# Optimization experiments

Hardware: AMD Instinct MI355X
Metric: run time of the kernel (lower is better)

The kernel has to match this reference:

```python
import jax, jax.numpy as jnp
import numpy as np

H = 256  # hidden_dim
Z = 4    # z_dim

def gru_step(x, h, Wih, Whh, bih, bhh):
    gi = x @ Wih.T + bih            # [B, 3H]
    gh = h @ Whh.T + bhh            # [B, 3H]
    ir, iz, inn = jnp.split(gi, 3, axis=-1)
    hr, hz, hn = jnp.split(gh, 3, axis=-1)
    r = jax.nn.sigmoid(ir + hr)
    z = jax.nn.sigmoid(iz + hz)
    n = jnp.tanh(inn + r * hn)
    return (1.0 - z) * n + z * h

def gru_scan(xs, h0, Wih, Whh, bih, bhh):
    # xs: [L, B, D] time-major; returns all hidden states [L, B, H]
    def step(h, x):
        h = gru_step(x, h, Wih, Whh, bih, bhh)
        return h, h
    _, hs = jax.lax.scan(step, h0, xs)
    return hs

def feat_z(z, fz_W1, fz_b1, fz_W2, fz_b2):
    # MLPEmbedding(z_dim -> [z_dim//2] -> feature_z), Linear+tanh per layer (dropout off in eval)
    h = jnp.tanh(z @ fz_W1.T + fz_b1)
    return jnp.tanh(h @ fz_W2.T + fz_b2)

def _make_params(key):
    ks = jax.random.split(key, 32)
    s = 0.05
    p = {}
    p['fx_W'] = jax.random.normal(ks[0], (64, 1)) * s
    p['fx_b'] = jnp.zeros((64,))
    p['fz_W1'] = jax.random.normal(ks[1], (2, 4)) * s
    p['fz_b1'] = jnp.zeros((2,))
    p['fz_W2'] = jax.random.normal(ks[2], (32, 2)) * s
    p['fz_b2'] = jnp.zeros((32,))
    p['phi1_Wih'] = jax.random.normal(ks[3], (3 * H, 64)) * s
    p['phi1_Whh'] = jax.random.normal(ks[4], (3 * H, H)) * s
    p['phi1_bih'] = jnp.zeros((3 * H,))
    p['phi1_bhh'] = jnp.zeros((3 * H,))
    p['phi2_Wih'] = jax.random.normal(ks[5], (3 * H, 32)) * s
    p['phi2_Whh'] = jax.random.normal(ks[6], (3 * H, H)) * s
    p['phi2_bih'] = jnp.zeros((3 * H,))
    p['phi2_bhh'] = jnp.zeros((3 * H,))
    p['pn_locW'] = jax.random.normal(ks[7], (Z, 2 * H)) * s
    p['pn_locb'] = jnp.zeros((Z,))
    p['pn_scaleW'] = jax.random.normal(ks[8], (Z, 2 * H)) * s
    p['pn_scaleb'] = jnp.zeros((Z,))
    p['th_Wih'] = jax.random.normal(ks[9], (3 * H, 32)) * s
    p['th_Whh'] = jax.random.normal(ks[10], (3 * H, H)) * s
    p['th_bih'] = jnp.zeros((3 * H,))
    p['th_bhh'] = jnp.zeros((3 * H,))
    p['tn_locW'] = jax.random.normal(ks[11], (1, H)) * s
    p['tn_locb'] = jnp.zeros((1,))
    return p

def setup_inputs() -> dict:
    key = jax.random.key(0)
    kx, ke, kp = jax.random.split(key, 3)
    B, L = 256, 512
    inp = {
        'x': jax.random.normal(kx, (B, L, 1), dtype=jnp.float32),
        'eps': jax.random.normal(ke, (L, B, Z), dtype=jnp.float32),
    }
    inp.update(_make_params(kp))
    return inp

def reference(x, eps, fx_W, fx_b, fz_W1, fz_b1, fz_W2, fz_b2,
              phi1_Wih, phi1_Whh, phi1_bih, phi1_bhh,
              phi2_Wih, phi2_Whh, phi2_bih, phi2_bhh,
              pn_locW, pn_locb, pn_scaleW, pn_scaleb,
              th_Wih, th_Whh, th_bih, th_bhh,
              tn_locW, tn_locb):
    B, L, _ = x.shape
    # ---- encode ----
    xf = jnp.tanh(x @ fx_W.T + fx_b)                 # [B, L, 64] feature_extra_x
    xs_rev = jnp.transpose(xf[:, ::-1, :], (1, 0, 2))  # [L, B, 64] reversed, time-major
    h0 = jnp.zeros((B, H), dtype=x.dtype)
    xh = gru_scan(xs_rev, h0, phi1_Wih, phi1_Whh, phi1_bih, phi1_bhh)  # [L, B, H]
    xh_r = xh[::-1]                                  # flip back to forward time order

    def enc_step(carry, inp_t):
        zh, zf = carry
        xh_t, eps_t = inp_t
        zh = gru_step(zf, zh, phi2_Wih, phi2_Whh, phi2_bih, phi2_bhh)
        cat = jnp.concatenate([zh, xh_t], axis=-1)   # [B, 2H]
        z_loc = cat @ pn_locW.T + pn_locb
        z_scale = jax.nn.softplus(cat @ pn_scaleW.T + pn_scaleb)
        z_t = z_loc + z_scale * eps_t                # Normal sample (n_sample=1 -> mean == sample)
        zf = feat_z(z_t, fz_W1, fz_b1, fz_W2, fz_b2)
        return (zh, zf), z_t

    zf0 = jnp.zeros((B, 32), dtype=x.dtype)
    _, z_tm = jax.lax.scan(enc_step, (h0, zf0), (xh_r, eps))  # [L, B, Z]

    # ---- decode ----
    zf_seq = feat_z(z_tm, fz_W1, fz_b1, fz_W2, fz_b2)          # [L, B, 32]
    hs = gru_scan(zf_seq, h0, th_Wih, th_Whh, th_bih, th_bhh)  # [L, B, H]
    x_loc = hs @ tn_locW.T + tn_locb                           # [L, B, 1]
    return jnp.transpose(x_loc, (1, 0, 2))                     # [B, L, 1]
```

## Files before the change

kernel.cpp:

```cpp
#include <hip/hip_runtime.h>
#include <hip/hip_bf16.h>
#include <stdint.h>


struct RvaeParams {
  const float *x, *eps;
  const float *fx_W, *fx_b;
  const float *fz_W1, *fz_b1, *fz_W2, *fz_b2;
  const float *p1_Wih, *p1_Whh, *p1_bih, *p1_bhh;
  const float *p2_Wih, *p2_Whh, *p2_bih, *p2_bhh;
  const float *pn_locW, *pn_locb, *pn_scaleW, *pn_scaleb;
  const float *th_Wih, *th_Whh, *th_bih, *th_bhh;
  const float *tn_locW, *tn_locb;
  float* out;
  unsigned* ctr;
  float* hbuf;
  float* zpart;
  float* zf_seq;
  __hip_bfloat16* xh;
};

__device__ __forceinline__ float agent_load_f32(const float* p) {
  return __hip_atomic_load(p, __ATOMIC_RELAXED, __HIP_MEMORY_SCOPE_AGENT);
}
__device__ __forceinline__ void agent_store_f32(float* p, float v) {
  __hip_atomic_store(p, v, __ATOMIC_RELAXED, __HIP_MEMORY_SCOPE_AGENT);
}
__device__ __forceinline__ unsigned long long agent_load_u64(const unsigned long long* p) {
  return __hip_atomic_load(p, __ATOMIC_RELAXED, __HIP_MEMORY_SCOPE_AGENT);
}
__device__ __forceinline__ float sigm(float xx) { return 1.0f / (1.0f + __expf(-xx)); }
__device__ __forceinline__ float ftanh(float xx) { return 1.0f - 2.0f / (__expf(2.0f * xx) + 1.0f); }
__device__ __forceinline__ float softplusf(float xx) { return (xx > 15.0f) ? xx : log1pf(__expf(xx)); }

__device__ __forceinline__ void gh_part(const float* Wh, const float* hL, int b, int u,
                                        float& ar, float& az, float& an) {
  float r0 = 0.f, z0 = 0.f, n0 = 0.f;
  const float4* h4 = (const float4*)hL + b * 65;
  const float4* wr = (const float4*)Wh + u * 65;
  const float4* wz = (const float4*)Wh + (32 + u) * 65;
  const float4* wn = (const float4*)Wh + (64 + u) * 65;
#pragma unroll 4
  for (int k = 0; k < 64; ++k) {
    float4 hv = h4[k];
    float4 a = wr[k]; float4 c = wz[k]; float4 d = wn[k];
    r0 = fmaf(a.x, hv.x, r0); r0 = fmaf(a.y, hv.y, r0); r0 = fmaf(a.z, hv.z, r0); r0 = fmaf(a.w, hv.w, r0);
    z0 = fmaf(c.x, hv.x, z0); z0 = fmaf(c.y, hv.y, z0); z0 = fmaf(c.z, hv.z, z0); z0 = fmaf(c.w, hv.w, z0);
    n0 = fmaf(d.x, hv.x, n0); n0 = fmaf(d.y, hv.y, n0); n0 = fmaf(d.z, hv.z, n0); n0 = fmaf(d.w, hv.w, n0);
  }
  ar = r0; az = z0; an = n0;
}

template<int KD4>
__device__ __forceinline__ void gi_part(const float* Wi, int strideF4, const float* inL, int b, int u,
                                        float& gr, float& gz, float& gn) {
  float r0 = 0.f, z0 = 0.f, n0 = 0.f;
  const float4* i4 = (const float4*)inL + b * 17;
  const float4* wr = (const float4*)Wi + u * strideF4;
  const float4* wz = (const float4*)Wi + (32 + u) * strideF4;
  const float4* wn = (const float4*)Wi + (64 + u) * strideF4;
#pragma unroll 4
  for (int k = 0; k < KD4; ++k) {
    float4 hv = i4[k];
    float4 a = wr[k]; float4 c = wz[k]; float4 d = wn[k];
    r0 = fmaf(a.x, hv.x, r0); r0 = fmaf(a.y, hv.y, r0); r0 = fmaf(a.z, hv.z, r0); r0 = fmaf(a.w, hv.w, r0);
    z0 = fmaf(c.x, hv.x, z0); z0 = fmaf(c.y, hv.y, z0); z0 = fmaf(c.z, hv.z, z0); z0 = fmaf(c.w, hv.w, z0);
    n0 = fmaf(d.x, hv.x, n0); n0 = fmaf(d.y, hv.y, n0); n0 = fmaf(d.z, hv.z, n0); n0 = fmaf(d.w, hv.w, n0);
  }
  gr = r0; gz = z0; gn = n0;
}

extern "C" __global__ void __launch_bounds__(256, 1) rvae_main(RvaeParams P) {
  __shared__ __align__(16) float Wh[96 * 260];
  __shared__ __align__(16) float SB[7584];
  __shared__ __align__(16) float hL[8 * 260];
  __shared__ __align__(16) float inL[8 * 68];
  __shared__ float bihL[96], bhhL[96];
  __shared__ float fxwL[64], fxbL[64];
  __shared__ float fzW1L[8], fzb1L[2], fzW2L[64], fzb2L[32];
  __shared__ float pnlb[4], pnsb[4];
  __shared__ float wred[4 * 8 * 8];
  __shared__ float zred[64];
  __shared__ float ztL[32];
  __shared__ float hmL[16];
  __shared__ float oredL[4 * 8];
  __shared__ float tnwL[32];
  __shared__ unsigned bcount;

  const int tid = threadIdx.x;
  const int wgid = blockIdx.x;
  const int s = wgid >> 5;
  const int g = wgid & 31;
  const int b_l = tid & 7;
  const int u = tid >> 3;
  const int j = s * 32 + u;
  const int bg = g * 8 + b_l;
  unsigned* gctr = P.ctr + g * 16;

  if (tid < 64) { fxwL[tid] = P.fx_W[tid]; fxbL[tid] = P.fx_b[tid]; fzW2L[tid] = P.fz_W2[tid]; }
  if (tid < 8)  fzW1L[tid] = P.fz_W1[tid];
  if (tid < 2)  fzb1L[tid] = P.fz_b1[tid];
  if (tid < 32) fzb2L[tid] = P.fz_b2[tid];
  if (tid < 4)  { pnlb[tid] = P.pn_locb[tid]; pnsb[tid] = P.pn_scaleb[tid]; }
  if (tid == 0) bcount = 0;

  auto gbar = [&]() {
    __syncthreads();
    if (tid == 0) {
      unsigned target = (++bcount) * 8u;
      __hip_atomic_fetch_add(gctr, 1u, __ATOMIC_RELEASE, __HIP_MEMORY_SCOPE_AGENT);
      int guard = 0;
      while (__hip_atomic_load(gctr, __ATOMIC_ACQUIRE, __HIP_MEMORY_SCOPE_AGENT) < target) {
        __builtin_amdgcn_s_sleep(1);
        if (++guard > (1 << 27)) break;
      }
    }
    __syncthreads();
  };

  auto load_whh = [&](const float* Whh) {
    for (int rr = 0; rr < 96; ++rr) {
      int gate = rr >> 5, uu = rr & 31;
      Wh[rr * 260 + tid] = Whh[(gate * 256 + s * 32 + uu) * 256 + tid];
    }
  };
  auto load_wih32 = [&](const float* Wih) {
    for (int blk = 0; blk < 12; ++blk) {
      int rr = blk * 8 + (tid >> 5); int c = tid & 31;
      int gate = rr >> 5, uu = rr & 31;
      SB[rr * 36 + c] = Wih[(gate * 256 + s * 32 + uu) * 32 + c];
    }
  };
  auto load_bias = [&](const float* bih, const float* bhh) {
    if (tid < 96) {
      int gate = tid >> 5, uu = tid & 31;
      bihL[tid] = bih[gate * 256 + s * 32 + uu];
      bhhL[tid] = bhh[gate * 256 + s * 32 + uu];
    }
  };

  load_whh(P.p1_Whh);
  for (int blk = 0; blk < 24; ++blk) {
    int rr = blk * 4 + (tid >> 6); int c = tid & 63;
    int gate = rr >> 5, uu = rr & 31;
    SB[rr * 68 + c] = P.p1_Wih[(gate * 256 + s * 32 + uu) * 64 + c];
  }
  load_bias(P.p1_bih, P.p1_bhh);
  agent_store_f32(P.hbuf + bg * 256 + j, 0.0f);
  {
#pragma unroll
    for (int i = 0; i < 2; ++i) {
      int idx = tid + i * 256; int bb = idx >> 6, k = idx & 63;
      float xv = P.x[(size_t)(g * 8 + bb) * 512 + 511];
      inL[bb * 68 + k] = ftanh(fmaf(xv, fxwL[k], fxbL[k]));
    }
  }
  gbar();
  for (int t = 0; t < 512; ++t) {
    const float* hin = P.hbuf + (t & 1) * 65536 + g * 2048;
    float* hout = P.hbuf + ((t + 1) & 1) * 65536;
    unsigned long long hv[4];
    const unsigned long long* h64 = (const unsigned long long*)hin;
#pragma unroll
    for (int i = 0; i < 4; ++i) hv[i] = agent_load_u64(h64 + tid + i * 256);
    float gr, gz, gn;
    gi_part<16>(SB, 17, inL, b_l, u, gr, gz, gn);
#pragma unroll
    for (int i = 0; i < 4; ++i) {
      int idx = tid + i * 256; int bb = idx >> 7, kp = (idx & 127) * 2;
      union { unsigned long long q; float f[2]; } cv; cv.q = hv[i];
      hL[bb * 260 + kp] = cv.f[0]; hL[bb * 260 + kp + 1] = cv.f[1];
    }
    __syncthreads();
    float ar, az, an;
    gh_part(Wh, hL, b_l, u, ar, az, an);
    float hold = hL[b_l * 260 + j];
    float r = sigm(gr + bihL[u] + ar + bhhL[u]);
    float z = sigm(gz + bihL[32 + u] + az + bhhL[32 + u]);
    float n = ftanh(fmaf(r, an + bhhL[64 + u], gn + bihL[64 + u]));
    float hnew = fmaf(z, hold - n, n);
    int t_in = 511 - t;
    agent_store_f32(hout + bg * 256 + j, hnew);
    P.xh[((size_t)wgid * 512 + t_in) * 256 + b_l * 32 + u] = __float2bfloat16(hnew);
    if (t < 511) {
#pragma unroll
      for (int i = 0; i < 2; ++i) {
        int idx = tid + i * 256; int bb = idx >> 6, k = idx & 63;
        float xv = P.x[(size_t)(g * 8 + bb) * 512 + (t_in - 1)];
        inL[bb * 68 + k] = ftanh(fmaf(xv, fxwL[k], fxbL[k]));
      }
    }
    gbar();
  }

  __syncthreads();
  load_whh(P.p2_Whh);
  load_wih32(P.p2_Wih);
  for (int idx = tid; idx < 2048; idx += 256) {
    int o = idx >> 9, c = idx & 511;
    SB[3456 + o * 516 + c] = P.pn_locW[idx];
    SB[5520 + o * 516 + c] = P.pn_scaleW[idx];
  }
  load_bias(P.p2_bih, P.p2_bhh);
  agent_store_f32(P.hbuf + bg * 256 + j, 0.0f);
  for (int idx = tid; idx < 8 * 68; idx += 256) inL[idx] = 0.0f;
  gbar();
  for (int t = 0; t < 512; ++t) {
    const float* hin = P.hbuf + (t & 1) * 65536 + g * 2048;
    float* hout = P.hbuf + ((t + 1) & 1) * 65536;
    unsigned long long hv[4];
    const unsigned long long* h64 = (const unsigned long long*)hin;
#pragma unroll
    for (int i = 0; i < 4; ++i) hv[i] = agent_load_u64(h64 + tid + i * 256);
    float xhv = __bfloat162float(P.xh[((size_t)wgid * 512 + t) * 256 + b_l * 32 + u]);
    float gr, gz, gn;
    gi_part<8>(SB, 9, inL, b_l, u, gr, gz, gn);
#pragma unroll
    for (int i = 0; i < 4; ++i) {
      int idx = tid + i * 256; int bb = idx >> 7, kp = (idx & 127) * 2;
      union { unsigned long long q; float f[2]; } cv; cv.q = hv[i];
      hL[bb * 260 + kp] = cv.f[0]; hL[bb * 260 + kp + 1] = cv.f[1];
    }
    __syncthreads();
    float ar, az, an;
    gh_part(Wh, hL, b_l, u, ar, az, an);
    float hold = hL[b_l * 260 + j];
    float r = sigm(gr + bihL[u] + ar + bhhL[u]);
    float z = sigm(gz + bihL[32 + u] + az + bhhL[32 + u]);
    float n = ftanh(fmaf(r, an + bhhL[64 + u], gn + bihL[64 + u]));
    float hnew = fmaf(z, hold - n, n);
    agent_store_f32(hout + bg * 256 + j, hnew);
    float p[8];
#pragma unroll
    for (int o = 0; o < 4; ++o)
      p[o] = fmaf(hnew, SB[3456 + o * 516 + j], xhv * SB[3456 + o * 516 + 256 + j]);
#pragma unroll
    for (int o = 0; o < 4; ++o)
      p[4 + o] = fmaf(hnew, SB[5520 + o * 516 + j], xhv * SB[5520 + o * 516 + 256 + j]);
#pragma unroll
    for (int o = 0; o < 8; ++o) {
      float v = p[o];
      v += __shfl_down(v, 32); v += __shfl_down(v, 16); v += __shfl_down(v, 8);
      p[o] = v;
    }
    {
      int lane = tid & 63, wv = tid >> 6;
      if (lane < 8) {
#pragma unroll
        for (int o = 0; o < 8; ++o) wred[wv * 64 + lane * 8 + o] = p[o];
      }
    }
    __syncthreads();
    float* zp = P.zpart + (t & 1) * 16384 + g * 512;
    if (tid < 64) {
      int bb = tid >> 3, o = tid & 7;
      float sum = wred[bb * 8 + o] + wred[64 + bb * 8 + o] + wred[128 + bb * 8 + o] + wred[192 + bb * 8 + o];
      agent_store_f32(zp + s * 64 + bb * 8 + o, sum);
    }
    gbar();
    if (tid < 64) {
      int bb = tid >> 3, o = tid & 7;
      float sum = 0.f;
#pragma unroll
      for (int sp = 0; sp < 8; ++sp) sum += agent_load_f32(zp + sp * 64 + bb * 8 + o);
      zred[bb * 8 + o] = sum;
    }
    __syncthreads();
    if (tid < 32) {
      int bb = tid >> 2, zi = tid & 3;
      float loc = zred[bb * 8 + zi] + pnlb[zi];
      float sc = softplusf(zred[bb * 8 + 4 + zi] + pnsb[zi]);
      float e = P.eps[((size_t)t * 256 + g * 8 + bb) * 4 + zi];
      ztL[bb * 4 + zi] = fmaf(sc, e, loc);
    }
    __syncthreads();
    if (tid < 16) {
      int bb = tid >> 1, m = tid & 1;
      float a = fzb1L[m];
#pragma unroll
      for (int i = 0; i < 4; ++i) a = fmaf(ztL[bb * 4 + i], fzW1L[m * 4 + i], a);
      hmL[bb * 2 + m] = ftanh(a);
    }
    __syncthreads();
    {
      int bb = tid >> 5, o = tid & 31;
      float zf = ftanh(fmaf(hmL[bb * 2], fzW2L[o * 2], fmaf(hmL[bb * 2 + 1], fzW2L[o * 2 + 1], fzb2L[o])));
      inL[bb * 68 + o] = zf;
      if (s == 0) agent_store_f32(P.zf_seq + ((size_t)t * 256 + g * 8 + bb) * 32 + o, zf);
    }
    __syncthreads();
  }

  __syncthreads();
  load_whh(P.th_Whh);
  load_wih32(P.th_Wih);
  load_bias(P.th_bih, P.th_bhh);
  if (tid < 32) tnwL[tid] = P.tn_locW[s * 32 + tid];
  agent_store_f32(P.hbuf + bg * 256 + j, 0.0f);
  gbar();
  const float tnb = P.tn_locb[0];
  for (int t = 0; t < 512; ++t) {
    const float* hin = P.hbuf + (t & 1) * 65536 + g * 2048;
    float* hout = P.hbuf + ((t + 1) & 1) * 65536;
    unsigned long long hv[4];
    const unsigned long long* h64 = (const unsigned long long*)hin;
#pragma unroll
    for (int i = 0; i < 4; ++i) hv[i] = agent_load_u64(h64 + tid + i * 256);
    {
      int bb = tid >> 5, o = tid & 31;
      inL[bb * 68 + o] = agent_load_f32(P.zf_seq + ((size_t)t * 256 + g * 8 + bb) * 32 + o);
    }
#pragma unroll
    for (int i = 0; i < 4; ++i) {
      int idx = tid + i * 256; int bb = idx >> 7, kp = (idx & 127) * 2;
      union { unsigned long long q; float f[2]; } cv; cv.q = hv[i];
      hL[bb * 260 + kp] = cv.f[0]; hL[bb * 260 + kp + 1] = cv.f[1];
    }
    __syncthreads();
    float gr, gz, gn;
    gi_part<8>(SB, 9, inL, b_l, u, gr, gz, gn);
    float ar, az, an;
    gh_part(Wh, hL, b_l, u, ar, az, an);
    float hold = hL[b_l * 260 + j];
    float r = sigm(gr + bihL[u] + ar + bhhL[u]);
    float z = sigm(gz + bihL[32 + u] + az + bhhL[32 + u]);
    float n = ftanh(fmaf(r, an + bhhL[64 + u], gn + bihL[64 + u]));
    float hnew = fmaf(z, hold - n, n);
    agent_store_f32(hout + bg * 256 + j, hnew);
    float pv = hnew * tnwL[u];
    pv += __shfl_down(pv, 32); pv += __shfl_down(pv, 16); pv += __shfl_down(pv, 8);
    {
      int lane = tid & 63, wv = tid >> 6;
      if (lane < 8) oredL[wv * 8 + lane] = pv;
    }
    __syncthreads();
    if (tid < 8) {
      float v = oredL[tid] + oredL[8 + tid] + oredL[16 + tid] + oredL[24 + tid];
      if (s == 0) v += tnb;
      atomicAdd(P.out + (size_t)(g * 8 + tid) * 512 + t, v);
    }
    gbar();
  }
}

extern "C" void kernel_launch(void* const* d_in, const int* in_sizes, int n_in,
                              void* d_out, int out_size, void* d_ws, size_t ws_size,
                              hipStream_t stream) {
  (void)in_sizes; (void)n_in; (void)ws_size;
  RvaeParams P;
  P.x        = (const float*)d_in[0];
  P.eps      = (const float*)d_in[1];
  P.fx_W     = (const float*)d_in[2];  P.fx_b     = (const float*)d_in[3];
  P.fz_W1    = (const float*)d_in[4];  P.fz_b1    = (const float*)d_in[5];
  P.fz_W2    = (const float*)d_in[6];  P.fz_b2    = (const float*)d_in[7];
  P.p1_Wih   = (const float*)d_in[8];  P.p1_Whh   = (const float*)d_in[9];
  P.p1_bih   = (const float*)d_in[10]; P.p1_bhh   = (const float*)d_in[11];
  P.p2_Wih   = (const float*)d_in[12]; P.p2_Whh   = (const float*)d_in[13];
  P.p2_bih   = (const float*)d_in[14]; P.p2_bhh   = (const float*)d_in[15];
  P.pn_locW  = (const float*)d_in[16]; P.pn_locb  = (const float*)d_in[17];
  P.pn_scaleW= (const float*)d_in[18]; P.pn_scaleb= (const float*)d_in[19];
  P.th_Wih   = (const float*)d_in[20]; P.th_Whh   = (const float*)d_in[21];
  P.th_bih   = (const float*)d_in[22]; P.th_bhh   = (const float*)d_in[23];
  P.tn_locW  = (const float*)d_in[24]; P.tn_locb  = (const float*)d_in[25];
  P.out = (float*)d_out;
  char* ws = (char*)d_ws;
  P.ctr    = (unsigned*)ws;
  P.hbuf   = (float*)(ws + 4096);
  P.zpart  = (float*)(ws + 4096 + 524288);
  P.zf_seq = (float*)(ws + 4096 + 524288 + 131072);
  P.xh = (__hip_bfloat16*)(ws + 4096 + 524288 + 131072 + 16777216);

  hipMemsetAsync(d_out, 0, (size_t)out_size * sizeof(float), stream);
  hipMemsetAsync(d_ws, 0, 4096, stream);
  void* args[] = { (void*)&P };
  hipError_t err = hipLaunchCooperativeKernel((void*)rvae_main, dim3(256), dim3(256), args, 0, stream);
  if (err != hipSuccess) {
    hipLaunchKernelGGL(rvae_main, dim3(256), dim3(256), 0, stream, P);
  }
}
```

Baseline: 12.78 ms.

## Rewrite RVAE kernel with per-slice flag sync, 512 threads, split-K gates

Replaces the counter-based group barrier with per-slice monotonic flags that each wave polls, so the two barriers per encoder step become one publish/poll. Block size doubles to 512 with a split-K GRU matvec reduced through DPP. The encoder's cross-block z reduction is dropped: every block computes the full loc/scale projection itself from staged xh and h, lagged one step. Other changes: packed bf16 xh stores, a shared LDS pool, and overlapping the decoder output reduction with the next step. The cost is more redundant per-block work and more LDS traffic.

```diff
diff --git a/kernel.cpp b/kernel.cpp
--- a/kernel.cpp
+++ b/kernel.cpp
@@ -2,6 +2,9 @@
 #include <hip/hip_bf16.h>
 #include <stdint.h>
 
+
+#define EXTF 11840
+#define POOLF (24576 + EXTF)
 
 struct RvaeParams {
   const float *x, *eps;
@@ -13,122 +16,100 @@
   const float *th_Wih, *th_Whh, *th_bih, *th_bhh;
   const float *tn_locW, *tn_locb;
   float* out;
-  unsigned* ctr;
+  unsigned* flags;
   float* hbuf;
-  float* zpart;
   float* zf_seq;
-  __hip_bfloat16* xh;
+  unsigned* xh;
 };
 
 __device__ __forceinline__ float agent_load_f32(const float* p) {
   return __hip_atomic_load(p, __ATOMIC_RELAXED, __HIP_MEMORY_SCOPE_AGENT);
 }
+__device__ __forceinline__ unsigned agent_load_u32(const unsigned* p) {
+  return __hip_atomic_load(p, __ATOMIC_RELAXED, __HIP_MEMORY_SCOPE_AGENT);
+}
+__device__ __forceinline__ unsigned long long agent_load_u64(const unsigned long long* p) {
+  return __hip_atomic_load(p, __ATOMIC_RELAXED, __HIP_MEMORY_SCOPE_AGENT);
+}
 __device__ __forceinline__ void agent_store_f32(float* p, float v) {
   __hip_atomic_store(p, v, __ATOMIC_RELAXED, __HIP_MEMORY_SCOPE_AGENT);
 }
-__device__ __forceinline__ unsigned long long agent_load_u64(const unsigned long long* p) {
-  return __hip_atomic_load(p, __ATOMIC_RELAXED, __HIP_MEMORY_SCOPE_AGENT);
-}
-__device__ __forceinline__ float sigm(float xx) { return 1.0f / (1.0f + __expf(-xx)); }
-__device__ __forceinline__ float ftanh(float xx) { return 1.0f - 2.0f / (__expf(2.0f * xx) + 1.0f); }
-__device__ __forceinline__ float softplusf(float xx) { return (xx > 15.0f) ? xx : log1pf(__expf(xx)); }
-
-__device__ __forceinline__ void gh_part(const float* Wh, const float* hL, int b, int u,
-                                        float& ar, float& az, float& an) {
-  float r0 = 0.f, z0 = 0.f, n0 = 0.f;
-  const float4* h4 = (const float4*)hL + b * 65;
-  const float4* wr = (const float4*)Wh + u * 65;
-  const float4* wz = (const float4*)Wh + (32 + u) * 65;
-  const float4* wn = (const float4*)Wh + (64 + u) * 65;
-#pragma unroll 4
-  for (int k = 0; k < 64; ++k) {
-    float4 hv = h4[k];
-    float4 a = wr[k]; float4 c = wz[k]; float4 d = wn[k];
-    r0 = fmaf(a.x, hv.x, r0); r0 = fmaf(a.y, hv.y, r0); r0 = fmaf(a.z, hv.z, r0); r0 = fmaf(a.w, hv.w, r0);
-    z0 = fmaf(c.x, hv.x, z0); z0 = fmaf(c.y, hv.y, z0); z0 = fmaf(c.z, hv.z, z0); z0 = fmaf(c.w, hv.w, z0);
-    n0 = fmaf(d.x, hv.x, n0); n0 = fmaf(d.y, hv.y, n0); n0 = fmaf(d.z, hv.z, n0); n0 = fmaf(d.w, hv.w, n0);
-  }
-  ar = r0; az = z0; an = n0;
-}
-
-template<int KD4>
-__device__ __forceinline__ void gi_part(const float* Wi, int strideF4, const float* inL, int b, int u,
-                                        float& gr, float& gz, float& gn) {
-  float r0 = 0.f, z0 = 0.f, n0 = 0.f;
-  const float4* i4 = (const float4*)inL + b * 17;
-  const float4* wr = (const float4*)Wi + u * strideF4;
-  const float4* wz = (const float4*)Wi + (32 + u) * strideF4;
-  const float4* wn = (const float4*)Wi + (64 + u) * strideF4;
-#pragma unroll 4
-  for (int k = 0; k < KD4; ++k) {
-    float4 hv = i4[k];
-    float4 a = wr[k]; float4 c = wz[k]; float4 d = wn[k];
-    r0 = fmaf(a.x, hv.x, r0); r0 = fmaf(a.y, hv.y, r0); r0 = fmaf(a.z, hv.z, r0); r0 = fmaf(a.w, hv.w, r0);
-    z0 = fmaf(c.x, hv.x, z0); z0 = fmaf(c.y, hv.y, z0); z0 = fmaf(c.z, hv.z, z0); z0 = fmaf(c.w, hv.w, z0);
-    n0 = fmaf(d.x, hv.x, n0); n0 = fmaf(d.y, hv.y, n0); n0 = fmaf(d.z, hv.z, n0); n0 = fmaf(d.w, hv.w, n0);
-  }
-  gr = r0; gz = z0; gn = n0;
-}
-
-extern "C" __global__ void __launch_bounds__(256, 1) rvae_main(RvaeParams P) {
-  __shared__ __align__(16) float Wh[96 * 260];
-  __shared__ __align__(16) float SB[7584];
-  __shared__ __align__(16) float hL[8 * 260];
-  __shared__ __align__(16) float inL[8 * 68];
+__device__ __forceinline__ void agent_store_u32(unsigned* p, unsigned v) {
+  __hip_atomic_store(p, v, __ATOMIC_RELAXED, __HIP_MEMORY_SCOPE_AGENT);
+}
+__device__ __forceinline__ float sigm(float v) { return 1.0f / (1.0f + __expf(-v)); }
+__device__ __forceinline__ float ftanh(float v) { return 1.0f - 2.0f / (__expf(2.0f * v) + 1.0f); }
+__device__ __forceinline__ float softplusf(float v) { return (v > 15.0f) ? v : log1pf(__expf(v)); }
+__device__ __forceinline__ unsigned f2bf(float x) {
+  unsigned uu = __float_as_uint(x);
+  return (uu + 0x7fffu + ((uu >> 16) & 1u)) >> 16;
+}
+template<int CTRL>
+__device__ __forceinline__ float dpp_add(float v) {
+  int xi = __builtin_amdgcn_update_dpp(0, __float_as_int(v), CTRL, 0xF, 0xF, true);
+  return v + __int_as_float(xi);
+}
+__device__ __forceinline__ float dpp_xor1_add(float v) {
+  int xi = __builtin_amdgcn_update_dpp(0, __float_as_int(v), 0xB1, 0xF, 0xF, true);
+  return v + __int_as_float(xi);
+}
+
+extern "C" __global__ void __launch_bounds__(512, 2) rvae_main(RvaeParams P) {
+  __shared__ __align__(16) float POOL[POOLF];
   __shared__ float bihL[96], bhhL[96];
   __shared__ float fxwL[64], fxbL[64];
   __shared__ float fzW1L[8], fzb1L[2], fzW2L[64], fzb2L[32];
-  __shared__ float pnlb[4], pnsb[4];
-  __shared__ float wred[4 * 8 * 8];
-  __shared__ float zred[64];
-  __shared__ float ztL[32];
-  __shared__ float hmL[16];
-  __shared__ float oredL[4 * 8];
-  __shared__ float tnwL[32];
-  __shared__ unsigned bcount;
+  __shared__ float pnlb[4], pnsb[4], tnwL[32];
+  __shared__ float pvL[8 * 36];
 
   const int tid = threadIdx.x;
   const int wgid = blockIdx.x;
-  const int s = wgid >> 5;
-  const int g = wgid & 31;
-  const int b_l = tid & 7;
-  const int u = tid >> 3;
-  const int j = s * 32 + u;
-  const int bg = g * 8 + b_l;
-  unsigned* gctr = P.ctr + g * 16;
+  const int s = wgid >> 5, g = wgid & 31;
+  const int u = tid >> 4, bq = (tid >> 1) & 7, kh = tid & 1;
+  const int lane = tid & 63;
+  float* Wh = POOL;
+  float* EXT = POOL + 24576;
+  unsigned* gflags = P.flags + g * 8;
 
   if (tid < 64) { fxwL[tid] = P.fx_W[tid]; fxbL[tid] = P.fx_b[tid]; fzW2L[tid] = P.fz_W2[tid]; }
   if (tid < 8)  fzW1L[tid] = P.fz_W1[tid];
   if (tid < 2)  fzb1L[tid] = P.fz_b1[tid];
-  if (tid < 32) fzb2L[tid] = P.fz_b2[tid];
+  if (tid < 32) { fzb2L[tid] = P.fz_b2[tid]; tnwL[tid] = P.tn_locW[s * 32 + tid]; }
   if (tid < 4)  { pnlb[tid] = P.pn_locb[tid]; pnsb[tid] = P.pn_scaleb[tid]; }
-  if (tid == 0) bcount = 0;
-
-  auto gbar = [&]() {
-    __syncthreads();
-    if (tid == 0) {
-      unsigned target = (++bcount) * 8u;
-      __hip_atomic_fetch_add(gctr, 1u, __ATOMIC_RELEASE, __HIP_MEMORY_SCOPE_AGENT);
-      int guard = 0;
-      while (__hip_atomic_load(gctr, __ATOMIC_ACQUIRE, __HIP_MEMORY_SCOPE_AGENT) < target) {
-        __builtin_amdgcn_s_sleep(1);
-        if (++guard > (1 << 27)) break;
-      }
-    }
-    __syncthreads();
-  };
-
-  auto load_whh = [&](const float* Whh) {
-    for (int rr = 0; rr < 96; ++rr) {
-      int gate = rr >> 5, uu = rr & 31;
-      Wh[rr * 260 + tid] = Whh[(gate * 256 + s * 32 + uu) * 256 + tid];
-    }
-  };
-  auto load_wih32 = [&](const float* Wih) {
-    for (int blk = 0; blk < 12; ++blk) {
-      int rr = blk * 8 + (tid >> 5); int c = tid & 31;
-      int gate = rr >> 5, uu = rr & 31;
-      SB[rr * 36 + c] = Wih[(gate * 256 + s * 32 + uu) * 32 + c];
+
+  auto poll = [&](unsigned tag) {
+    int guard = 0;
+    for (;;) {
+      unsigned f = agent_load_u32(gflags + (lane & 7));
+      if (__all((int)(f >= tag))) break;
+      __builtin_amdgcn_s_sleep(1);
+      if (++guard > (1 << 20)) break;
+    }
+  };
+  auto publish = [&](unsigned tag) {
+    asm volatile("s_waitcnt vmcnt(0)" ::: "memory");
+    __syncthreads();
+    if (tid == 0) agent_store_u32(gflags + s, tag);
+  };
+  auto load_Wh = [&](const float* Whh) {
+    for (int i = tid; i < 6144; i += 512) {
+      int r = i >> 6, c4 = (i & 63) << 2, gate = r >> 5, uu = r & 31;
+      *(float4*)(Wh + r * 256 + c4) =
+          *(const float4*)(Whh + (size_t)(gate * 256 + s * 32 + uu) * 256 + c4);
+    }
+  };
+  auto load_Wi64 = [&](const float* Wih) {
+    for (int i = tid; i < 1536; i += 512) {
+      int r = i >> 4, c4 = (i & 15) << 2, gate = r >> 5, uu = r & 31;
+      *(float4*)(EXT + r * 64 + c4) =
+          *(const float4*)(Wih + (size_t)(gate * 256 + s * 32 + uu) * 64 + c4);
+    }
+  };
+  auto load_Wi32 = [&](const float* Wih) {
+    for (int i = tid; i < 768; i += 512) {
+      int r = i >> 3, c4 = (i & 7) << 2, gate = r >> 5, uu = r & 31;
+      *(float4*)(EXT + r * 32 + c4) =
+          *(const float4*)(Wih + (size_t)(gate * 256 + s * 32 + uu) * 32 + c4);
     }
   };
   auto load_bias = [&](const float* bih, const float* bhh) {
@@ -138,208 +119,223 @@
       bhhL[tid] = bhh[gate * 256 + s * 32 + uu];
     }
   };
-
-  load_whh(P.p1_Whh);
-  for (int blk = 0; blk < 24; ++blk) {
-    int rr = blk * 4 + (tid >> 6); int c = tid & 63;
-    int gate = rr >> 5, uu = rr & 31;
-    SB[rr * 68 + c] = P.p1_Wih[(gate * 256 + s * 32 + uu) * 64 + c];
+  auto h_issue = [&](int par, unsigned long long& qa, unsigned long long& qb) {
+    const unsigned long long* hb =
+        (const unsigned long long*)(P.hbuf + par * 65536 + g * 2048) + tid * 2;
+    qa = agent_load_u64(hb); qb = agent_load_u64(hb + 1);
+  };
+  auto h_write = [&](float* hLp, unsigned long long qa, unsigned long long qb, bool zero) {
+    int row = tid >> 6, k0 = (tid & 63) << 2;
+    float4 v;
+    if (zero) { v = make_float4(0.f, 0.f, 0.f, 0.f); }
+    else {
+      union { unsigned long long q[2]; float f[4]; } cv; cv.q[0] = qa; cv.q[1] = qb;
+      v = *(float4*)cv.f;
+    }
+    *(float4*)(hLp + row * 260 + k0) = v;
+  };
+  auto gi = [&](const float* inLp, int K, int stride, float& gr, float& gz, float& gn) {
+    int k0 = kh * (K >> 1);
+    const float4* iv = (const float4*)(inLp + bq * stride + k0);
+    const float4* wr = (const float4*)(EXT + u * K + k0);
+    const float4* wz = (const float4*)(EXT + 32 * K + u * K + k0);
+    const float4* wn = (const float4*)(EXT + 64 * K + u * K + k0);
+    float r = 0.f, z = 0.f, n = 0.f;
+    int nc = K >> 3;
+#pragma unroll 4
+    for (int c = 0; c < nc; ++c) {
+      float4 hv = iv[c], a = wr[c], b2 = wz[c], d = wn[c];
+      r = fmaf(a.x, hv.x, r); r = fmaf(a.y, hv.y, r); r = fmaf(a.z, hv.z, r); r = fmaf(a.w, hv.w, r);
+      z = fmaf(b2.x, hv.x, z); z = fmaf(b2.y, hv.y, z); z = fmaf(b2.z, hv.z, z); z = fmaf(b2.w, hv.w, z);
+      n = fmaf(d.x, hv.x, n); n = fmaf(d.y, hv.y, n); n = fmaf(d.z, hv.z, n); n = fmaf(d.w, hv.w, n);
+    }
+    gr = r; gz = z; gn = n;
+  };
+  auto gru_core = [&](float* hLp, float gir, float giz, float gin, int outPar) -> float {
+    const float4* hp = (const float4*)(hLp + bq * 260 + kh * 128);
+    const float4* wr = (const float4*)(Wh + u * 256 + kh * 128);
+    const float4* wz = (const float4*)(Wh + 8192 + u * 256 + kh * 128);
+    const float4* wn = (const float4*)(Wh + 16384 + u * 256 + kh * 128);
+    float ar = gir, az = giz, an = 0.f;
+#pragma unroll 8
+    for (int c = 0; c < 32; ++c) {
+      float4 hv = hp[c];
+      float4 a = wr[c], b2 = wz[c], d = wn[c];
+      ar = fmaf(a.x, hv.x, ar); ar = fmaf(a.y, hv.y, ar);
+      ar = fmaf(a.z, hv.z, ar); ar = fmaf(a.w, hv.w, ar);
+      az = fmaf(b2.x, hv.x, az); az = fmaf(b2.y, hv.y, az);
+      az = fmaf(b2.z, hv.z, az); az = fmaf(b2.w, hv.w, az);
+      an = fmaf(d.x, hv.x, an); an = fmaf(d.y, hv.y, an);
+      an = fmaf(d.z, hv.z, an); an = fmaf(d.w, hv.w, an);
+    }
+    ar = dpp_xor1_add(ar); az = dpp_xor1_add(az);
+    float ani = dpp_xor1_add(gin); an = dpp_xor1_add(an);
+    float rr = sigm(ar + bihL[u] + bhhL[u]);
+    float zz = sigm(az + bihL[32 + u] + bhhL[32 + u]);
+    float nn = ftanh(fmaf(rr, an + bhhL[64 + u], ani + bihL[64 + u]));
+    float hold = hLp[bq * 260 + s * 32 + u];
+    float hnew = fmaf(zz, hold - nn, nn);
+    if (kh == 0)
+      agent_store_f32(P.hbuf + outPar * 65536 + (g * 8 + bq) * 256 + s * 32 + u, hnew);
+    return hnew;
+  };
+
+  load_Wh(P.p1_Whh); load_Wi64(P.p1_Wih); load_bias(P.p1_bih, P.p1_bhh);
+  {
+    float* inL1 = EXT + 6144;
+    float* hL1  = EXT + 6688;
+    __syncthreads();
+    { int bb = tid >> 6, k = tid & 63;
+      float xv = P.x[(size_t)(g * 8 + bb) * 512 + 511];
+      inL1[bb * 68 + k] = ftanh(fmaf(xv, fxwL[k], fxbL[k])); }
+    __syncthreads();
+#pragma unroll 1
+    for (int t = 0; t < 512; ++t) {
+      unsigned long long qa = 0, qb = 0;
+      if (t) { poll(t); h_issue(t & 1, qa, qb); }
+      float gr, gz, gn;
+      gi(inL1, 64, 68, gr, gz, gn);
+      h_write(hL1, qa, qb, t == 0);
+      __syncthreads();
+      float hnew = gru_core(hL1, gr, gz, gn, (t + 1) & 1);
+      int t_in = 511 - t;
+      {
+        float hp2 = __shfl_xor(hnew, 16);
+        if (kh == 0 && (u & 1) == 0) {
+          unsigned pk = f2bf(hnew) | (f2bf(hp2) << 16);
+          agent_store_u32(P.xh + (size_t)t_in * 32768 + (g * 8 + bq) * 128 + s * 16 + (u >> 1), pk);
+        }
+      }
+      if (t < 511) {
+        int bb = tid >> 6, k = tid & 63;
+        float xv = P.x[(size_t)(g * 8 + bb) * 512 + (t_in - 1)];
+        inL1[bb * 68 + k] = ftanh(fmaf(xv, fxwL[k], fxbL[k]));
+      }
+      publish(t + 1);
+    }
   }
-  load_bias(P.p1_bih, P.p1_bhh);
-  agent_store_f32(P.hbuf + bg * 256 + j, 0.0f);
+
+  load_Wh(P.p2_Whh); load_Wi32(P.p2_Wih); load_bias(P.p2_bih, P.p2_bhh);
   {
+    float* SBp  = EXT + 3072;
+    float* xhL  = EXT + 7232;
+    float* inL2 = EXT + 9344;
+    float* hL2  = EXT + 9632;
+    float* pL   = EXT + 11712;
+    float* hmL2 = EXT + 11784;
+    for (int i = tid; i < 2048; i += 512) {
+      int o = i >> 9, c = i & 511;
+      SBp[o * 520 + c] = P.pn_locW[i];
+      SBp[(4 + o) * 520 + c] = P.pn_scaleW[i];
+    }
+    for (int i = tid; i < 288; i += 512) inL2[i] = 0.f;
+    poll(512);
+    __syncthreads();
+    auto stage_xh_w = [&](unsigned xa, unsigned xb) {
+      int w0 = tid, w1 = tid + 512;
+      xhL[(w0 >> 7) * 264 + ((w0 & 127) << 1)]     = __uint_as_float((xa & 0xffffu) << 16);
+      xhL[(w0 >> 7) * 264 + ((w0 & 127) << 1) + 1] = __uint_as_float(xa & 0xffff0000u);
+      xhL[(w1 >> 7) * 264 + ((w1 & 127) << 1)]     = __uint_as_float((xb & 0xffffu) << 16);
+      xhL[(w1 >> 7) * 264 + ((w1 & 127) << 1) + 1] = __uint_as_float(xb & 0xffff0000u);
+    };
+    auto pblock = [&](int tp, bool toIn) {
+      {
+        int b = tid >> 6, o = (tid >> 3) & 7, c = tid & 7;
+        const float* base = (c < 4) ? (hL2 + b * 260 + c * 64) : (xhL + b * 264 + (c - 4) * 64);
+        const float* wrow = SBp + o * 520 + c * 64;
+        float acc = 0.f;
 #pragma unroll
-    for (int i = 0; i < 2; ++i) {
-      int idx = tid + i * 256; int bb = idx >> 6, k = idx & 63;
-      float xv = P.x[(size_t)(g * 8 + bb) * 512 + 511];
-      inL[bb * 68 + k] = ftanh(fmaf(xv, fxwL[k], fxbL[k]));
+        for (int m = 0; m < 16; ++m) {
+          int mi = ((m + 2 * c) & 15) << 2;
+          float4 v = *(const float4*)(base + mi);
+          float4 w = *(const float4*)(wrow + mi);
+          acc = fmaf(v.x, w.x, fmaf(v.y, w.y, fmaf(v.z, w.z, fmaf(v.w, w.w, acc))));
+        }
+        acc = dpp_add<0x111>(acc); acc = dpp_add<0x112>(acc); acc = dpp_add<0x114>(acc);
+        if (c == 7) pL[b * 9 + o] = acc;
+      }
+      __syncthreads();
+      if (tid < 16) {
+        int bb = tid >> 1, m = tid & 1;
+        float a = fzb1L[m];
+#pragma unroll
+        for (int zi = 0; zi < 4; ++zi) {
+          float loc = pL[bb * 9 + zi] + pnlb[zi];
+          float sc = softplusf(pL[bb * 9 + 4 + zi] + pnsb[zi]);
+          float e = P.eps[((size_t)tp * 256 + g * 8 + bb) * 4 + zi];
+          a = fmaf(fmaf(sc, e, loc), fzW1L[m * 4 + zi], a);
+        }
+        hmL2[bb * 2 + m] = ftanh(a);
+      }
+      __syncthreads();
+      if (tid < 256) {
+        int bb = tid >> 5, o = tid & 31;
+        float zf = ftanh(fmaf(hmL2[bb * 2], fzW2L[o * 2],
+                         fmaf(hmL2[bb * 2 + 1], fzW2L[o * 2 + 1], fzb2L[o])));
+        if (toIn) inL2[bb * 36 + o] = zf;
+        if (s == 0) agent_store_f32(P.zf_seq + ((size_t)tp * 256 + g * 8 + bb) * 32 + o, zf);
+      }
+      __syncthreads();
+    };
+#pragma unroll 1
+    for (int t = 0; t < 512; ++t) {
+      unsigned long long qa = 0, qb = 0; unsigned xa = 0, xb = 0;
+      if (t) {
+        poll(1024 + t);
+        h_issue(t & 1, qa, qb);
+        const unsigned* xp = P.xh + (size_t)(t - 1) * 32768 + g * 1024;
+        xa = agent_load_u32(xp + tid); xb = agent_load_u32(xp + tid + 512);
+      }
+      h_write(hL2, qa, qb, t == 0);
+      if (t) stage_xh_w(xa, xb);
+      __syncthreads();
+      if (t) pblock(t - 1, true);
+      float gr, gz, gn;
+      gi(inL2, 32, 36, gr, gz, gn);
+      gru_core(hL2, gr, gz, gn, (t + 1) & 1);
+      publish(1024 + t + 1);
+    }
+    {
+      poll(1536);
+      unsigned long long qa, qb; h_issue(0, qa, qb);
+      const unsigned* xp = P.xh + (size_t)511 * 32768 + g * 1024;
+      unsigned xa = agent_load_u32(xp + tid), xb = agent_load_u32(xp + tid + 512);
+      h_write(hL2, qa, qb, false);
+      stage_xh_w(xa, xb);
+      __syncthreads();
+      pblock(511, false);
+      __syncthreads();
     }
   }
-  gbar();
-  for (int t = 0; t < 512; ++t) {
-    const float* hin = P.hbuf + (t & 1) * 65536 + g * 2048;
-    float* hout = P.hbuf + ((t + 1) & 1) * 65536;
-    unsigned long long hv[4];
-    const unsigned long long* h64 = (const unsigned long long*)hin;
-#pragma unroll
-    for (int i = 0; i < 4; ++i) hv[i] = agent_load_u64(h64 + tid + i * 256);
-    float gr, gz, gn;
-    gi_part<16>(SB, 17, inL, b_l, u, gr, gz, gn);
-#pragma unroll
-    for (int i = 0; i < 4; ++i) {
-      int idx = tid + i * 256; int bb = idx >> 7, kp = (idx & 127) * 2;
-      union { unsigned long long q; float f[2]; } cv; cv.q = hv[i];
-      hL[bb * 260 + kp] = cv.f[0]; hL[bb * 260 + kp + 1] = cv.f[1];
-    }
-    __syncthreads();
-    float ar, az, an;
-    gh_part(Wh, hL, b_l, u, ar, az, an);
-    float hold = hL[b_l * 260 + j];
-    float r = sigm(gr + bihL[u] + ar + bhhL[u]);
-    float z = sigm(gz + bihL[32 + u] + az + bhhL[32 + u]);
-    float n = ftanh(fmaf(r, an + bhhL[64 + u], gn + bihL[64 + u]));
-    float hnew = fmaf(z, hold - n, n);
-    int t_in = 511 - t;
-    agent_store_f32(hout + bg * 256 + j, hnew);
-    P.xh[((size_t)wgid * 512 + t_in) * 256 + b_l * 32 + u] = __float2bfloat16(hnew);
-    if (t < 511) {
-#pragma unroll
-      for (int i = 0; i < 2; ++i) {
-        int idx = tid + i * 256; int bb = idx >> 6, k = idx & 63;
-        float xv = P.x[(size_t)(g * 8 + bb) * 512 + (t_in - 1)];
-        inL[bb * 68 + k] = ftanh(fmaf(xv, fxwL[k], fxbL[k]));
-      }
-    }
-    gbar();
-  }
-
-  __syncthreads();
-  load_whh(P.p2_Whh);
-  load_wih32(P.p2_Wih);
-  for (int idx = tid; idx < 2048; idx += 256) {
-    int o = idx >> 9, c = idx & 511;
-    SB[3456 + o * 516 + c] = P.pn_locW[idx];
-    SB[5520 + o * 516 + c] = P.pn_scaleW[idx];
-  }
-  load_bias(P.p2_bih, P.p2_bhh);
-  agent_store_f32(P.hbuf + bg * 256 + j, 0.0f);
-  for (int idx = tid; idx < 8 * 68; idx += 256) inL[idx] = 0.0f;
-  gbar();
-  for (int t = 0; t < 512; ++t) {
-    const float* hin = P.hbuf + (t & 1) * 65536 + g * 2048;
-    float* hout = P.hbuf + ((t + 1) & 1) * 65536;
-    unsigned long long hv[4];
-    const unsigned long long* h64 = (const unsigned long long*)hin;
-#pragma unroll
-    for (int i = 0; i < 4; ++i) hv[i] = agent_load_u64(h64 + tid + i * 256);
-    float xhv = __bfloat162float(P.xh[((size_t)wgid * 512 + t) * 256 + b_l * 32 + u]);
-    float gr, gz, gn;
-    gi_part<8>(SB, 9, inL, b_l, u, gr, gz, gn);
-#pragma unroll
-    for (int i = 0; i < 4; ++i) {
-      int idx = tid + i * 256; int bb = idx >> 7, kp = (idx & 127) * 2;
-      union { unsigned long long q; float f[2]; } cv; cv.q = hv[i];
-      hL[bb * 260 + kp] = cv.f[0]; hL[bb * 260 + kp + 1] = cv.f[1];
-    }
-    __syncthreads();
-    float ar, az, an;
-    gh_part(Wh, hL, b_l, u, ar, az, an);
-    float hold = hL[b_l * 260 + j];
-    float r = sigm(gr + bihL[u] + ar + bhhL[u]);
-    float z = sigm(gz + bihL[32 + u] + az + bhhL[32 + u]);
-    float n = ftanh(fmaf(r, an + bhhL[64 + u], gn + bihL[64 + u]));
-    float hnew = fmaf(z, hold - n, n);
-    agent_store_f32(hout + bg * 256 + j, hnew);
-    float p[8];
-#pragma unroll
-    for (int o = 0; o < 4; ++o)
-      p[o] = fmaf(hnew, SB[3456 + o * 516 + j], xhv * SB[3456 + o * 516 + 256 + j]);
-#pragma unroll
-    for (int o = 0; o < 4; ++o)
-      p[4 + o] = fmaf(hnew, SB[5520 + o * 516 + j], xhv * SB[5520 + o * 516 + 256 + j]);
-#pragma unroll
-    for (int o = 0; o < 8; ++o) {
-      float v = p[o];
-      v += __shfl_down(v, 32); v += __shfl_down(v, 16); v += __shfl_down(v, 8);
-      p[o] = v;
-    }
-    {
-      int lane = tid & 63, wv = tid >> 6;
-      if (lane < 8) {
-#pragma unroll
-        for (int o = 0; o < 8; ++o) wred[wv * 64 + lane * 8 + o] = p[o];
-      }
-    }
-    __syncthreads();
-    float* zp = P.zpart + (t & 1) * 16384 + g * 512;
-    if (tid < 64) {
-      int bb = tid >> 3, o = tid & 7;
-      float sum = wred[bb * 8 + o] + wred[64 + bb * 8 + o] + wred[128 + bb * 8 + o] + wred[192 + bb * 8 + o];
-      agent_store_f32(zp + s * 64 + bb * 8 + o, sum);
-    }
-    gbar();
-    if (tid < 64) {
-      int bb = tid >> 3, o = tid & 7;
-      float sum = 0.f;
-#pragma unroll
-      for (int sp = 0; sp < 8; ++sp) sum += agent_load_f32(zp + sp * 64 + bb * 8 + o);
-      zred[bb * 8 + o] = sum;
-    }
-    __syncthreads();
-    if (tid < 32) {
-      int bb = tid >> 2, zi = tid & 3;
-      float loc = zred[bb * 8 + zi] + pnlb[zi];
-      float sc = softplusf(zred[bb * 8 + 4 + zi] + pnsb[zi]);
-      float e = P.eps[((size_t)t * 256 + g * 8 + bb) * 4 + zi];
-      ztL[bb * 4 + zi] = fmaf(sc, e, loc);
-    }
-    __syncthreads();
-    if (tid < 16) {
-      int bb = tid >> 1, m = tid & 1;
-      float a = fzb1L[m];
-#pragma unroll
-      for (int i = 0; i < 4; ++i) a = fmaf(ztL[bb * 4 + i], fzW1L[m * 4 + i], a);
-      hmL[bb * 2 + m] = ftanh(a);
-    }
-    __syncthreads();
-    {
-      int bb = tid >> 5, o = tid & 31;
-      float zf = ftanh(fmaf(hmL[bb * 2], fzW2L[o * 2], fmaf(hmL[bb * 2 + 1], fzW2L[o * 2 + 1], fzb2L[o])));
-      inL[bb * 68 + o] = zf;
-      if (s == 0) agent_store_f32(P.zf_seq + ((size_t)t * 256 + g * 8 + bb) * 32 + o, zf);
-    }
-    __syncthreads();
-  }
-
-  __syncthreads();
-  load_whh(P.th_Whh);
-  load_wih32(P.th_Wih);
-  load_bias(P.th_bih, P.th_bhh);
-  if (tid < 32) tnwL[tid] = P.tn_locW[s * 32 + tid];
-  agent_store_f32(P.hbuf + bg * 256 + j, 0.0f);
-  gbar();
-  const float tnb = P.tn_locb[0];
-  for (int t = 0; t < 512; ++t) {
-    const float* hin = P.hbuf + (t & 1) * 65536 + g * 2048;
-    float* hout = P.hbuf + ((t + 1) & 1) * 65536;
-    unsigned long long hv[4];
-    const unsigned long long* h64 = (const unsigned long long*)hin;
-#pragma unroll
-    for (int i = 0; i < 4; ++i) hv[i] = agent_load_u64(h64 + tid + i * 256);
-    {
-      int bb = tid >> 5, o = tid & 31;
-      inL[bb * 68 + o] = agent_load_f32(P.zf_seq + ((size_t)t * 256 + g * 8 + bb) * 32 + o);
-    }
-#pragma unroll
-    for (int i = 0; i < 4; ++i) {
-      int idx = tid + i * 256; int bb = idx >> 7, kp = (idx & 127) * 2;
-      union { unsigned long long q; float f[2]; } cv; cv.q = hv[i];
-      hL[bb * 260 + kp] = cv.f[0]; hL[bb * 260 + kp + 1] = cv.f[1];
-    }
-    __syncthreads();
-    float gr, gz, gn;
-    gi_part<8>(SB, 9, inL, b_l, u, gr, gz, gn);
-    float ar, az, an;
-    gh_part(Wh, hL, b_l, u, ar, az, an);
-    float hold = hL[b_l * 260 + j];
-    float r = sigm(gr + bihL[u] + ar + bhhL[u]);
-    float z = sigm(gz + bihL[32 + u] + az + bhhL[32 + u]);
-    float n = ftanh(fmaf(r, an + bhhL[64 + u], gn + bihL[64 + u]));
-    float hnew = fmaf(z, hold - n, n);
-    agent_store_f32(hout + bg * 256 + j, hnew);
-    float pv = hnew * tnwL[u];
-    pv += __shfl_down(pv, 32); pv += __shfl_down(pv, 16); pv += __shfl_down(pv, 8);
-    {
-      int lane = tid & 63, wv = tid >> 6;
-      if (lane < 8) oredL[wv * 8 + lane] = pv;
-    }
-    __syncthreads();
-    if (tid < 8) {
-      float v = oredL[tid] + oredL[8 + tid] + oredL[16 + tid] + oredL[24 + tid];
-      if (s == 0) v += tnb;
-      atomicAdd(P.out + (size_t)(g * 8 + tid) * 512 + t, v);
-    }
-    gbar();
+
+  load_Wh(P.th_Whh); load_Wi32(P.th_Wih); load_bias(P.th_bih, P.th_bhh);
+  {
+    float* inL3 = EXT + 3072;
+    float* hL3  = EXT + 3360;
+    const float tnb = P.tn_locb[0];
+    __syncthreads();
+#pragma unroll 1
+    for (int t = 0; t < 512; ++t) {
+      float zfv = 0.f;
+      if (tid < 256)
+        zfv = agent_load_f32(P.zf_seq + ((size_t)t * 256 + g * 8 + (tid >> 5)) * 32 + (tid & 31));
+      unsigned long long qa = 0, qb = 0;
+      if (t) { poll(2048 + t); h_issue(t & 1, qa, qb); }
+      if (tid < 256) inL3[(tid >> 5) * 36 + (tid & 31)] = zfv;
+      h_write(hL3, qa, qb, t == 0);
+      __syncthreads();
+      float gr, gz, gn;
+      gi(inL3, 32, 36, gr, gz, gn);
+      float hnew = gru_core(hL3, gr, gz, gn, (t + 1) & 1);
+      if (kh == 0) pvL[bq * 36 + u] = hnew * tnwL[u];
+      publish(2048 + t + 1);
+      if (tid < 8) {
+        float acc = (s == 0) ? tnb : 0.f;
+#pragma unroll 8
+        for (int i = 0; i < 32; ++i) acc += pvL[tid * 36 + i];
+        atomicAdd(P.out + (size_t)(g * 8 + tid) * 512 + t, acc);
+      }
+    }
   }
 }
 
@@ -364,17 +360,16 @@
   P.tn_locW  = (const float*)d_in[24]; P.tn_locb  = (const float*)d_in[25];
   P.out = (float*)d_out;
   char* ws = (char*)d_ws;
-  P.ctr    = (unsigned*)ws;
+  P.flags  = (unsigned*)ws;
   P.hbuf   = (float*)(ws + 4096);
-  P.zpart  = (float*)(ws + 4096 + 524288);
-  P.zf_seq = (float*)(ws + 4096 + 524288 + 131072);
-  P.xh = (__hip_bfloat16*)(ws + 4096 + 524288 + 131072 + 16777216);
+  P.zf_seq = (float*)(ws + 4096 + 524288);
+  P.xh     = (unsigned*)(ws + 4096 + 524288 + 16777216);
 
   hipMemsetAsync(d_out, 0, (size_t)out_size * sizeof(float), stream);
   hipMemsetAsync(d_ws, 0, 4096, stream);
   void* args[] = { (void*)&P };
-  hipError_t err = hipLaunchCooperativeKernel((void*)rvae_main, dim3(256), dim3(256), args, 0, stream);
+  hipError_t err = hipLaunchCooperativeKernel((void*)rvae_main, dim3(256), dim3(512), args, 0, stream);
   if (err != hipSuccess) {
-    hipLaunchKernelGGL(rvae_main, dim3(256), dim3(256), 0, stream, P);
+    hipLaunchKernelGGL(rvae_main, dim3(256), dim3(512), 0, stream, P);
   }
 }
```

Result: slower. 15.18 ms (+18.7%).
